# Optimization experiments

Measured on AMD Instinct MI355X. Metric: run time of the kernel, lower is better.

Reference implementation:

```python
import jax, jax.numpy as jnp
import numpy as np

EPS = 1e-4

def setup_inputs() -> dict:
    key = jax.random.key(0)
    x = jax.random.normal(key, (32, 512, 4000), dtype=jnp.float32)
    return {"x": x}

def reference(x):
    # x: [batch, bins, frames]; causal cumulative normalization along frames
    frames = x.shape[-1]
    count = jnp.arange(1, frames + 1, dtype=x.dtype).reshape(1, 1, frames)
    cum_sum = jnp.cumsum(x, axis=-1)
    cum_pow_sum = jnp.cumsum(x * x, axis=-1)
    cum_mean = cum_sum / count
    cum_var = cum_pow_sum / count - cum_mean * cum_mean
    cum_std = jnp.sqrt(cum_var + EPS)
    return (x - cum_mean) / cum_std
```

## Files before the change

kernel.cpp:

```cpp
#include <hip/hip_runtime.h>

#define EPS 1e-4f
#define FRAMES 4000

__global__ __launch_bounds__(256) void cumnorm_kernel(const float* __restrict__ x,
                                                      float* __restrict__ out,
                                                      int rows) {
    const int wavesPerBlock = blockDim.x >> 6;
    const int row  = blockIdx.x * wavesPerBlock + (threadIdx.x >> 6);
    const int lane = threadIdx.x & 63;
    if (row >= rows) return;

    const float4* __restrict__ xr = (const float4*)(x + (size_t)row * FRAMES);
    float4* __restrict__ outr     = (float4*)(out + (size_t)row * FRAMES);

    const int nvec = FRAMES >> 2;
    float carry_s = 0.0f, carry_q = 0.0f;

    for (int base = 0; base < nvec; base += 64) {
        const int idx = base + lane;
        float4 v = make_float4(0.0f, 0.0f, 0.0f, 0.0f);
        if (idx < nvec) v = xr[idx];

        float s0 = v.x;
        float s1 = s0 + v.y;
        float s2 = s1 + v.z;
        float s3 = s2 + v.w;
        float q0 = v.x * v.x;
        float q1 = fmaf(v.y, v.y, q0);
        float q2 = fmaf(v.z, v.z, q1);
        float q3 = fmaf(v.w, v.w, q2);

        float ss = s3, qq = q3;
        #pragma unroll
        for (int d = 1; d < 64; d <<= 1) {
            float us = __shfl_up(ss, d, 64);
            float uq = __shfl_up(qq, d, 64);
            if (lane >= d) { ss += us; qq += uq; }
        }

        const float tot_s = __shfl(ss, 63, 64);
        const float tot_q = __shfl(qq, 63, 64);

        const float excl_s = (ss - s3) + carry_s;
        const float excl_q = (qq - q3) + carry_q;

        if (idx < nvec) {
            const float base_cnt = (float)(idx << 2);
            float4 r;
            {
                const float cs = excl_s + s0, cq = excl_q + q0;
                const float inv  = __builtin_amdgcn_rcpf(base_cnt + 1.0f);
                const float mean = cs * inv;
                const float var  = fmaf(-mean, mean, cq * inv);
                r.x = (v.x - mean) * __builtin_amdgcn_rsqf(var + EPS);
            }
            {
                const float cs = excl_s + s1, cq = excl_q + q1;
                const float inv  = __builtin_amdgcn_rcpf(base_cnt + 2.0f);
                const float mean = cs * inv;
                const float var  = fmaf(-mean, mean, cq * inv);
                r.y = (v.y - mean) * __builtin_amdgcn_rsqf(var + EPS);
            }
            {
                const float cs = excl_s + s2, cq = excl_q + q2;
                const float inv  = __builtin_amdgcn_rcpf(base_cnt + 3.0f);
                const float mean = cs * inv;
                const float var  = fmaf(-mean, mean, cq * inv);
                r.z = (v.z - mean) * __builtin_amdgcn_rsqf(var + EPS);
            }
            {
                const float cs = excl_s + s3, cq = excl_q + q3;
                const float inv  = __builtin_amdgcn_rcpf(base_cnt + 4.0f);
                const float mean = cs * inv;
                const float var  = fmaf(-mean, mean, cq * inv);
                r.w = (v.w - mean) * __builtin_amdgcn_rsqf(var + EPS);
            }
            outr[idx] = r;
        }

        carry_s += tot_s;
        carry_q += tot_q;
    }
}

extern "C" void kernel_launch(void* const* d_in, const int* in_sizes, int n_in,
                              void* d_out, int out_size, void* d_ws, size_t ws_size,
                              hipStream_t stream) {
    const float* x = (const float*)d_in[0];
    float* out = (float*)d_out;
    const int rows = in_sizes[0] / FRAMES;

    const int block = 256;
    const int rowsPerBlock = block / 64;
    const int grid = (rows + rowsPerBlock - 1) / rowsPerBlock;
    cumnorm_kernel<<<grid, block, 0, stream>>>(x, out, rows);
}
```

Before: 432.8 us.

## Process each row with a whole block using per-thread 16-element chunks

Each 4000-frame row now gets a full 256-thread block instead of one wave looping serially over 16 chunks. Each thread loads 16 contiguous elements, does a local serial scan, a wave shuffle scan, and a cross-wave combine through shared memory. This removes the serial loop-carried dependence per row and raises memory-level parallelism, at the cost of a __syncthreads, 6 idle threads per block, and strided rather than fully coalesced per-thread float4 loads.

```diff
diff --git a/kernel.cpp b/kernel.cpp
--- a/kernel.cpp
+++ b/kernel.cpp
@@ -2,85 +2,80 @@
 
 #define EPS 1e-4f
 #define FRAMES 4000
+#define EPT 16
+#define ACTIVE 250
 
 __global__ __launch_bounds__(256) void cumnorm_kernel(const float* __restrict__ x,
-                                                      float* __restrict__ out,
-                                                      int rows) {
-    const int wavesPerBlock = blockDim.x >> 6;
-    const int row  = blockIdx.x * wavesPerBlock + (threadIdx.x >> 6);
-    const int lane = threadIdx.x & 63;
-    if (row >= rows) return;
+                                                      float* __restrict__ out) {
+    const int row  = blockIdx.x;
+    const int t    = threadIdx.x;
+    const int lane = t & 63;
+    const int wave = t >> 6;
 
-    const float4* __restrict__ xr = (const float4*)(x + (size_t)row * FRAMES);
-    float4* __restrict__ outr     = (float4*)(out + (size_t)row * FRAMES);
+    __shared__ float wave_s[4];
+    __shared__ float wave_q[4];
 
-    const int nvec = FRAMES >> 2;
-    float carry_s = 0.0f, carry_q = 0.0f;
+    const float* __restrict__ xr  = x   + (size_t)row * FRAMES;
+    float*       __restrict__ outr = out + (size_t)row * FRAMES;
 
-    for (int base = 0; base < nvec; base += 64) {
-        const int idx = base + lane;
-        float4 v = make_float4(0.0f, 0.0f, 0.0f, 0.0f);
-        if (idx < nvec) v = xr[idx];
+    const bool active = (t < ACTIVE);
 
-        float s0 = v.x;
-        float s1 = s0 + v.y;
-        float s2 = s1 + v.z;
-        float s3 = s2 + v.w;
-        float q0 = v.x * v.x;
-        float q1 = fmaf(v.y, v.y, q0);
-        float q2 = fmaf(v.z, v.z, q1);
-        float q3 = fmaf(v.w, v.w, q2);
+    float v[EPT];
+    if (active) {
+        const float4* xp = (const float4*)(xr + t * EPT);
+        float4 a = xp[0], b = xp[1], c = xp[2], d = xp[3];
+        v[0]=a.x;  v[1]=a.y;  v[2]=a.z;  v[3]=a.w;
+        v[4]=b.x;  v[5]=b.y;  v[6]=b.z;  v[7]=b.w;
+        v[8]=c.x;  v[9]=c.y;  v[10]=c.z; v[11]=c.w;
+        v[12]=d.x; v[13]=d.y; v[14]=d.z; v[15]=d.w;
+    } else {
+        #pragma unroll
+        for (int j = 0; j < EPT; ++j) v[j] = 0.0f;
+    }
 
-        float ss = s3, qq = q3;
+    float ts = 0.0f, tq = 0.0f;
+    #pragma unroll
+    for (int j = 0; j < EPT; ++j) { ts += v[j]; tq = fmaf(v[j], v[j], tq); }
+
+    float ss = ts, qq = tq;
+    #pragma unroll
+    for (int d = 1; d < 64; d <<= 1) {
+        float us = __shfl_up(ss, d, 64);
+        float uq = __shfl_up(qq, d, 64);
+        if (lane >= d) { ss += us; qq += uq; }
+    }
+
+    if (lane == 63) { wave_s[wave] = ss; wave_q[wave] = qq; }
+    __syncthreads();
+    float base_s = 0.0f, base_q = 0.0f;
+    #pragma unroll
+    for (int w = 0; w < 3; ++w) {
+        if (w < wave) { base_s += wave_s[w]; base_q += wave_q[w]; }
+    }
+
+    const float excl_s = base_s + (ss - ts);
+    const float excl_q = base_q + (qq - tq);
+
+    if (active) {
+        float cs = excl_s, cq = excl_q;
+        const float cnt0 = (float)(t * EPT);
+        float4* op = (float4*)(outr + t * EPT);
         #pragma unroll
-        for (int d = 1; d < 64; d <<= 1) {
-            float us = __shfl_up(ss, d, 64);
-            float uq = __shfl_up(qq, d, 64);
-            if (lane >= d) { ss += us; qq += uq; }
-        }
-
-        const float tot_s = __shfl(ss, 63, 64);
-        const float tot_q = __shfl(qq, 63, 64);
-
-        const float excl_s = (ss - s3) + carry_s;
-        const float excl_q = (qq - q3) + carry_q;
-
-        if (idx < nvec) {
-            const float base_cnt = (float)(idx << 2);
+        for (int g = 0; g < 4; ++g) {
             float4 r;
-            {
-                const float cs = excl_s + s0, cq = excl_q + q0;
-                const float inv  = __builtin_amdgcn_rcpf(base_cnt + 1.0f);
+            float* rp = (float*)&r;
+            #pragma unroll
+            for (int k = 0; k < 4; ++k) {
+                const int j = g * 4 + k;
+                cs += v[j];
+                cq = fmaf(v[j], v[j], cq);
+                const float inv  = __builtin_amdgcn_rcpf(cnt0 + (float)(j + 1));
                 const float mean = cs * inv;
                 const float var  = fmaf(-mean, mean, cq * inv);
-                r.x = (v.x - mean) * __builtin_amdgcn_rsqf(var + EPS);
+                rp[k] = (v[j] - mean) * __builtin_amdgcn_rsqf(var + EPS);
             }
-            {
-                const float cs = excl_s + s1, cq = excl_q + q1;
-                const float inv  = __builtin_amdgcn_rcpf(base_cnt + 2.0f);
-                const float mean = cs * inv;
-                const float var  = fmaf(-mean, mean, cq * inv);
-                r.y = (v.y - mean) * __builtin_amdgcn_rsqf(var + EPS);
-            }
-            {
-                const float cs = excl_s + s2, cq = excl_q + q2;
-                const float inv  = __builtin_amdgcn_rcpf(base_cnt + 3.0f);
-                const float mean = cs * inv;
-                const float var  = fmaf(-mean, mean, cq * inv);
-                r.z = (v.z - mean) * __builtin_amdgcn_rsqf(var + EPS);
-            }
-            {
-                const float cs = excl_s + s3, cq = excl_q + q3;
-                const float inv  = __builtin_amdgcn_rcpf(base_cnt + 4.0f);
-                const float mean = cs * inv;
-                const float var  = fmaf(-mean, mean, cq * inv);
-                r.w = (v.w - mean) * __builtin_amdgcn_rsqf(var + EPS);
-            }
-            outr[idx] = r;
+            op[g] = r;
         }
-
-        carry_s += tot_s;
-        carry_q += tot_q;
     }
 }
 
@@ -91,8 +86,5 @@
     float* out = (float*)d_out;
     const int rows = in_sizes[0] / FRAMES;
 
-    const int block = 256;
-    const int rowsPerBlock = block / 64;
-    const int grid = (rows + rowsPerBlock - 1) / rowsPerBlock;
-    cumnorm_kernel<<<grid, block, 0, stream>>>(x, out, rows);
+    cumnorm_kernel<<<rows, 256, 0, stream>>>(x, out);
 }
```

Result: no change. 434.1 us (+0.3%).
